# Optimization experiments

Measured on AMD Instinct MI355X. Metric: run time of the kernel, lower is better.

The kernel has to match this reference:

```python
import jax, jax.numpy as jnp
from jax import lax
import numpy as np

B, C, H, W = 32, 128, 64, 64
OUT, KH, KW = 128, 3, 3
E, INTERM = 4, 256


def setup_inputs() -> dict:
    key = jax.random.key(0)
    k1, k2, k3, k4 = jax.random.split(key, 4)
    x = jax.random.normal(k1, (B, C, H, W), dtype=jnp.float32)
    routing_w = jax.random.normal(k2, (INTERM, C), dtype=jnp.float32) * 0.05
    routing_b = jax.random.normal(k3, (INTERM,), dtype=jnp.float32) * 0.05
    expert_weight = jax.random.normal(k4, (E, OUT * C * KH * KW), dtype=jnp.float32) * 0.05
    return {"x": x, "routing_w": routing_w, "routing_b": routing_b, "expert_weight": expert_weight}


def reference(x, routing_w, routing_b, expert_weight):
    b = x.shape[0]
    # adaptive_avg_pool2d(x, 1).flatten(1)
    pooled = x.mean(axis=(2, 3))                              # [B, C]
    rt = jax.nn.sigmoid(pooled @ routing_w.T + routing_b)     # [B, 256]
    # avg_pool1d kernel=stride=interm_d//num_experts
    routing = rt.reshape(b, E, INTERM // E).mean(axis=-1)     # [B, E]
    # CondConv2d: per-sample mixed kernels, grouped conv over batch
    w = routing @ expert_weight                               # [B, OUT*C*KH*KW]
    w = w.reshape(b * OUT, C, KH, KW)                         # OIHW, O grouped by sample
    xg = x.reshape(1, b * C, H, W)
    y = lax.conv_general_dilated(
        xg, w,
        window_strides=(1, 1),
        padding=((1, 1), (1, 1)),
        dimension_numbers=('NCHW', 'OIHW', 'NCHW'),
        feature_group_count=b,
    )
    return y.reshape(b, OUT, H, W)
```

## Files before the change

kernel.cpp:

```cpp
#include <hip/hip_runtime.h>

typedef __attribute__((ext_vector_type(8))) short short8;
typedef __attribute__((ext_vector_type(4))) float f32x4;

#define B_      32
#define C_      128
#define H_      64
#define W_      64
#define OUT_    128
#define PLANE   4096
#define EWSZ    147456

__device__ inline short f2bf(float f) {
    unsigned u = __builtin_bit_cast(unsigned, f);
    u += 0x7fff + ((u >> 16) & 1);
    return (short)(u >> 16);
}

__global__ void pool_kernel(const float* __restrict__ x, float* __restrict__ pooled) {
    const int bc = blockIdx.x;
    const float4* plane = (const float4*)(x + (size_t)bc * PLANE);
    float s = 0.f;
#pragma unroll
    for (int i = 0; i < 4; ++i) {
        float4 v = plane[threadIdx.x + i * 256];
        s += v.x + v.y + v.z + v.w;
    }
#pragma unroll
    for (int off = 32; off > 0; off >>= 1) s += __shfl_down(s, off);
    __shared__ float ls[4];
    const int wave = threadIdx.x >> 6, lane = threadIdx.x & 63;
    if (lane == 0) ls[wave] = s;
    __syncthreads();
    if (threadIdx.x == 0)
        pooled[bc] = (ls[0] + ls[1] + ls[2] + ls[3]) * (1.f / 4096.f);
}

__global__ void routing_kernel(const float* __restrict__ pooled,
                               const float* __restrict__ rw,
                               const float* __restrict__ rb,
                               float* __restrict__ routing) {
    const int b = blockIdx.x;
    __shared__ float ps[C_];
    if (threadIdx.x < C_) ps[threadIdx.x] = pooled[b * C_ + threadIdx.x];
    __syncthreads();
    const int i = threadIdx.x;
    const float4* w4 = (const float4*)(rw + (size_t)i * C_);
    float z = rb[i];
#pragma unroll 8
    for (int c4 = 0; c4 < 32; ++c4) {
        float4 wv = w4[c4];
        z += wv.x * ps[c4 * 4 + 0] + wv.y * ps[c4 * 4 + 1]
           + wv.z * ps[c4 * 4 + 2] + wv.w * ps[c4 * 4 + 3];
    }
    float s = 1.f / (1.f + expf(-z));
#pragma unroll
    for (int off = 32; off > 0; off >>= 1) s += __shfl_down(s, off);
    if ((threadIdx.x & 63) == 0)
        routing[b * 4 + (threadIdx.x >> 6)] = s * (1.f / 64.f);
}

__global__ void wgen_kernel(const float* __restrict__ routing,
                            const float* __restrict__ ew,
                            short* __restrict__ wbuf) {
    const int ct = blockIdx.x;
    const int cc = ct / 9, t = ct % 9;
    const int b = blockIdx.y;
    const int tid = threadIdx.x;
    const int mf = tid >> 6, l = tid & 63;
    const int o = mf * 16 + (l & 15);
    const int c0 = cc * 32 + ((l >> 4) << 3);
    const float r0 = routing[b * 4 + 0], r1 = routing[b * 4 + 1];
    const float r2 = routing[b * 4 + 2], r3 = routing[b * 4 + 3];
    const float* e0 = ew + (size_t)o * 1152 + (size_t)c0 * 9 + t;
    short8 v;
#pragma unroll
    for (int j = 0; j < 8; ++j) {
        const float* p = e0 + j * 9;
        float val = r0 * p[0] + r1 * p[EWSZ] + r2 * p[2 * EWSZ] + r3 * p[3 * EWSZ];
        v[j] = f2bf(val);
    }
    *(short8*)(wbuf + ((size_t)(b * 4 + cc) * 36864 + ((size_t)(t * 8 + mf) * 64 + l) * 8)) = v;
}

__global__ __launch_bounds__(512, 2) void conv_kernel(const float* __restrict__ x,
                                                      const short* __restrict__ wbuf,
                                                      float* __restrict__ out) {
    __shared__ __attribute__((aligned(16))) short ws_s[36864];
    __shared__ __attribute__((aligned(16))) short xs_s[26400];

    const int b = blockIdx.x, hb = blockIdx.y;
    const int h0 = hb * 8;
    const int tid = threadIdx.x;
    const int wid = tid >> 6, lane = tid & 63;
    const int ln15 = lane & 15, lg = lane >> 4;

    for (int i = tid; i < 13200; i += 512) ((int*)xs_s)[i] = 0;

    f32x4 acc[8][4];
#pragma unroll
    for (int m = 0; m < 8; ++m)
#pragma unroll
        for (int n = 0; n < 4; ++n) acc[m][n] = (f32x4){0.f, 0.f, 0.f, 0.f};

    const float* xb = x + (size_t)b * C_ * PLANE;
    const short* wsrc_b = wbuf + (size_t)b * 4 * 36864;

    int tw[5], tr[5], tcg[5], trow[5];
#pragma unroll
    for (int it = 0; it < 5; ++it) {
        const int task = it * 512 + tid;
        tw[it] = task & 63;
        const int rc = task >> 6;
        tr[it] = rc % 10;
        tcg[it] = rc / 10;
        trow[it] = h0 - 1 + tr[it];
    }

    float xpre[5][8];
#pragma unroll
    for (int it = 0; it < 5; ++it) {
        const bool valid = (unsigned)trow[it] < 64u;
        const float* src = xb + (size_t)(tcg[it] * 8) * PLANE + trow[it] * 64 + tw[it];
#pragma unroll
        for (int k = 0; k < 8; ++k)
            xpre[it][k] = valid ? src[(size_t)k * PLANE] : 0.f;
    }

    __syncthreads();

    for (int cc = 0; cc < 4; ++cc) {
#pragma unroll
        for (int it = 0; it < 5; ++it) {
            short8 v;
#pragma unroll
            for (int k = 0; k < 8; ++k) v[k] = f2bf(xpre[it][k]);
            *(short8*)&xs_s[((tr[it] * 66) + 1 + tw[it]) * 40 + tcg[it] * 8] = v;
        }
        {
            const char* srcb = (const char*)(wsrc_b + (size_t)cc * 36864);
            char* dstb = (char*)ws_s;
#pragma unroll
            for (int it = 0; it < 9; ++it) {
                const int off = (wid * 9 + it) * 1024 + lane * 16;
                __builtin_amdgcn_global_load_lds(
                    (const __attribute__((address_space(1))) void*)(srcb + off),
                    (__attribute__((address_space(3))) void*)(dstb + off), 16, 0, 0);
            }
        }
        __syncthreads();

        if (cc < 3) {
#pragma unroll
            for (int it = 0; it < 5; ++it) {
                const bool valid = (unsigned)trow[it] < 64u;
                const float* src = xb + (size_t)((cc + 1) * 32 + tcg[it] * 8) * PLANE
                                 + trow[it] * 64 + tw[it];
#pragma unroll
                for (int k = 0; k < 8; ++k)
                    xpre[it][k] = valid ? src[(size_t)k * PLANE] : 0.f;
            }
        }

#pragma unroll
        for (int t = 0; t < 9; ++t) {
            const int kh = t / 3, kw = t % 3;
            short8 bfr[4];
#pragma unroll
            for (int nf = 0; nf < 4; ++nf)
                bfr[nf] = *(const short8*)&xs_s[(((wid + kh) * 66) + nf * 16 + ln15 + kw) * 40 + lg * 8];
#pragma unroll
            for (int mf = 0; mf < 8; ++mf) {
                short8 af = *(const short8*)&ws_s[((t * 8 + mf) * 64 + lane) * 8];
#pragma unroll
                for (int nf = 0; nf < 4; ++nf)
                    acc[mf][nf] = __builtin_amdgcn_mfma_f32_16x16x32_bf16(
                        af, bfr[nf], acc[mf][nf], 0, 0, 0);
            }
        }
        __syncthreads();
    }

    float* ob = out + (size_t)b * OUT_ * PLANE;
    const int h = h0 + wid;
#pragma unroll
    for (int mf = 0; mf < 8; ++mf) {
#pragma unroll
        for (int nf = 0; nf < 4; ++nf) {
            const int w = nf * 16 + ln15;
            const int o0 = mf * 16 + lg * 4;
#pragma unroll
            for (int q = 0; q < 4; ++q)
                ob[((size_t)(o0 + q) * 64 + h) * 64 + w] = acc[mf][nf][q];
        }
    }
}

extern "C" void kernel_launch(void* const* d_in, const int* in_sizes, int n_in,
                              void* d_out, int out_size, void* d_ws, size_t ws_size,
                              hipStream_t stream) {
    const float* x  = (const float*)d_in[0];
    const float* rw = (const float*)d_in[1];
    const float* rb = (const float*)d_in[2];
    const float* ew = (const float*)d_in[3];
    float* out = (float*)d_out;

    float* pooled  = (float*)d_ws;
    float* routing = pooled + 4096;
    short* wbuf    = (short*)(pooled + 8192);

    pool_kernel<<<dim3(B_ * C_), 256, 0, stream>>>(x, pooled);
    routing_kernel<<<dim3(B_), 256, 0, stream>>>(pooled, rw, rb, routing);
    wgen_kernel<<<dim3(36, B_), 512, 0, stream>>>(routing, ew, wbuf);
    conv_kernel<<<dim3(B_, 8), 512, 0, stream>>>(x, wbuf, out);
}
```

Before: 189.4 us.

## Pre-pack expert weights, vectorize mixing, and shrink conv tiles for occupancy

A new kernel repacks the expert weights into the MFMA fragment layout once. A simpler vectorized mix kernel then blends the four experts per sample with coalesced loads, replacing the strided gather in the old weight generator. The conv kernel moves to 256 threads covering 4 output rows and uses a smaller LDS footprint. It stages the weight tile in two halves (taps 0-3, then 4-8) and converts the x prefetch to bf16 in registers, so more blocks fit per CU and the grid doubles. In exchange it adds an extra kernel launch and workspace traffic, more barriers per channel chunk, and each weight tile is reloaded by twice as many blocks.

After: 197.9 us. +4.5%, slower.

```diff
diff --git a/kernel.cpp b/kernel.cpp
--- a/kernel.cpp
+++ b/kernel.cpp
@@ -1,6 +1,7 @@
 #include <hip/hip_runtime.h>
 
 typedef __attribute__((ext_vector_type(8))) short short8;
+typedef __attribute__((ext_vector_type(4))) short shortv4;
 typedef __attribute__((ext_vector_type(4))) float f32x4;
 
 #define B_      32
@@ -60,42 +61,71 @@
         routing[b * 4 + (threadIdx.x >> 6)] = s * (1.f / 64.f);
 }
 
-__global__ void wgen_kernel(const float* __restrict__ routing,
-                            const float* __restrict__ ew,
+__global__ void epack_kernel(const float* __restrict__ ew, float* __restrict__ epk) {
+    const int os = blockIdx.x;
+    const int cc = blockIdx.y;
+    const int e  = blockIdx.z;
+    __shared__ float ls[16 * 292];
+    const int tid = threadIdx.x;
+
+    for (int idx = tid; idx < 1152; idx += 256) {
+        const int i = idx / 72, q = idx % 72;
+        float4 v = *(const float4*)(ew + (size_t)e * EWSZ
+                     + (size_t)(os * 16 + i) * 1152 + cc * 288 + q * 4);
+        *(float4*)&ls[i * 292 + q * 4] = v;
+    }
+    __syncthreads();
+
+    float* outp = epk + ((size_t)e * 4 + cc) * 36864;
+    for (int idx = tid; idx < 1152; idx += 256) {
+        const int t = idx / 128, r = idx % 128;
+        const int l = r >> 1, j0 = (r & 1) * 4;
+        const int row = l & 15, cb = (l >> 4) * 8 + j0;
+        float4 v;
+        v.x = ls[row * 292 + (cb + 0) * 9 + t];
+        v.y = ls[row * 292 + (cb + 1) * 9 + t];
+        v.z = ls[row * 292 + (cb + 2) * 9 + t];
+        v.w = ls[row * 292 + (cb + 3) * 9 + t];
+        *(float4*)(outp + (size_t)(t * 8 + os) * 512 + r * 4) = v;
+    }
+}
+
+__global__ void wmix_kernel(const float* __restrict__ rbuf,
+                            const float* __restrict__ epk,
                             short* __restrict__ wbuf) {
-    const int ct = blockIdx.x;
-    const int cc = ct / 9, t = ct % 9;
-    const int b = blockIdx.y;
-    const int tid = threadIdx.x;
-    const int mf = tid >> 6, l = tid & 63;
-    const int o = mf * 16 + (l & 15);
-    const int c0 = cc * 32 + ((l >> 4) << 3);
-    const float r0 = routing[b * 4 + 0], r1 = routing[b * 4 + 1];
-    const float r2 = routing[b * 4 + 2], r3 = routing[b * 4 + 3];
-    const float* e0 = ew + (size_t)o * 1152 + (size_t)c0 * 9 + t;
-    short8 v;
-#pragma unroll
-    for (int j = 0; j < 8; ++j) {
-        const float* p = e0 + j * 9;
-        float val = r0 * p[0] + r1 * p[EWSZ] + r2 * p[2 * EWSZ] + r3 * p[3 * EWSZ];
-        v[j] = f2bf(val);
-    }
-    *(short8*)(wbuf + ((size_t)(b * 4 + cc) * 36864 + ((size_t)(t * 8 + mf) * 64 + l) * 8)) = v;
-}
-
-__global__ __launch_bounds__(512, 2) void conv_kernel(const float* __restrict__ x,
+#pragma unroll
+    for (int it = 0; it < 2; ++it) {
+        const int idx = blockIdx.x * 512 + it * 256 + threadIdx.x;
+        const int b = idx / 36864;
+        const int r = idx - b * 36864;
+        const float r0 = rbuf[b * 4 + 0], r1 = rbuf[b * 4 + 1];
+        const float r2 = rbuf[b * 4 + 2], r3 = rbuf[b * 4 + 3];
+        float4 a = *(const float4*)(epk + (size_t)r * 4);
+        float4 bb = *(const float4*)(epk + 147456 + (size_t)r * 4);
+        float4 c = *(const float4*)(epk + 2 * 147456 + (size_t)r * 4);
+        float4 d = *(const float4*)(epk + 3 * 147456 + (size_t)r * 4);
+        shortv4 v;
+        v[0] = f2bf(r0 * a.x + r1 * bb.x + r2 * c.x + r3 * d.x);
+        v[1] = f2bf(r0 * a.y + r1 * bb.y + r2 * c.y + r3 * d.y);
+        v[2] = f2bf(r0 * a.z + r1 * bb.z + r2 * c.z + r3 * d.z);
+        v[3] = f2bf(r0 * a.w + r1 * bb.w + r2 * c.w + r3 * d.w);
+        *(shortv4*)(wbuf + (size_t)b * 147456 + (size_t)r * 4) = v;
+    }
+}
+
+__global__ __launch_bounds__(256, 2) void conv_kernel(const float* __restrict__ x,
                                                       const short* __restrict__ wbuf,
                                                       float* __restrict__ out) {
-    __shared__ __attribute__((aligned(16))) short ws_s[36864];
-    __shared__ __attribute__((aligned(16))) short xs_s[26400];
+    __shared__ __attribute__((aligned(16))) short xs_s[15840];
+    __shared__ __attribute__((aligned(16))) short ws_s[20480];
 
     const int b = blockIdx.x, hb = blockIdx.y;
-    const int h0 = hb * 8;
+    const int h0 = hb * 4;
     const int tid = threadIdx.x;
     const int wid = tid >> 6, lane = tid & 63;
     const int ln15 = lane & 15, lg = lane >> 4;
 
-    for (int i = tid; i < 13200; i += 512) ((int*)xs_s)[i] = 0;
+    for (int i = tid; i < 7920; i += 256) ((int*)xs_s)[i] = 0;
 
     f32x4 acc[8][4];
 #pragma unroll
@@ -106,78 +136,83 @@
     const float* xb = x + (size_t)b * C_ * PLANE;
     const short* wsrc_b = wbuf + (size_t)b * 4 * 36864;
 
-    int tw[5], tr[5], tcg[5], trow[5];
-#pragma unroll
-    for (int it = 0; it < 5; ++it) {
-        const int task = it * 512 + tid;
+    int tw[6], tr[6], tcg[6], trow[6];
+#pragma unroll
+    for (int it = 0; it < 6; ++it) {
+        const int task = it * 256 + tid;
         tw[it] = task & 63;
         const int rc = task >> 6;
-        tr[it] = rc % 10;
-        tcg[it] = rc / 10;
+        tr[it] = rc % 6;
+        tcg[it] = rc / 6;
         trow[it] = h0 - 1 + tr[it];
     }
 
-    float xpre[5][8];
-#pragma unroll
-    for (int it = 0; it < 5; ++it) {
-        const bool valid = (unsigned)trow[it] < 64u;
-        const float* src = xb + (size_t)(tcg[it] * 8) * PLANE + trow[it] * 64 + tw[it];
-#pragma unroll
-        for (int k = 0; k < 8; ++k)
-            xpre[it][k] = valid ? src[(size_t)k * PLANE] : 0.f;
-    }
-
+    short8 xpre[6];
+#define LOADX(CCC)                                                              \
+    {                                                                           \
+        _Pragma("unroll")                                                       \
+        for (int it = 0; it < 6; ++it) {                                        \
+            const bool valid = (unsigned)trow[it] < 64u;                        \
+            const float* src = xb + (size_t)((CCC) * 32 + tcg[it] * 8) * PLANE  \
+                             + trow[it] * 64 + tw[it];                          \
+            short8 v;                                                           \
+            _Pragma("unroll")                                                   \
+            for (int k = 0; k < 8; ++k)                                         \
+                v[k] = f2bf(valid ? src[(size_t)k * PLANE] : 0.f);              \
+            xpre[it] = v;                                                       \
+        }                                                                       \
+    }
+
+#define DO_TAP(TL, T)                                                           \
+    {                                                                           \
+        const int kh = (T) / 3, kw = (T) % 3;                                   \
+        short8 bfr[4];                                                          \
+        _Pragma("unroll")                                                       \
+        for (int nf = 0; nf < 4; ++nf)                                          \
+            bfr[nf] = *(const short8*)&xs_s[((wid + kh) * 66 + nf * 16 + ln15 + kw) * 40 + lg * 8]; \
+        _Pragma("unroll")                                                       \
+        for (int mf = 0; mf < 8; ++mf) {                                        \
+            short8 af = *(const short8*)&ws_s[(((TL) * 8 + mf) * 64 + lane) * 8]; \
+            _Pragma("unroll")                                                   \
+            for (int nf = 0; nf < 4; ++nf)                                      \
+                acc[mf][nf] = __builtin_amdgcn_mfma_f32_16x16x32_bf16(          \
+                    af, bfr[nf], acc[mf][nf], 0, 0, 0);                         \
+        }                                                                       \
+    }
+
+    LOADX(0);
     __syncthreads();
 
     for (int cc = 0; cc < 4; ++cc) {
 #pragma unroll
-        for (int it = 0; it < 5; ++it) {
-            short8 v;
-#pragma unroll
-            for (int k = 0; k < 8; ++k) v[k] = f2bf(xpre[it][k]);
-            *(short8*)&xs_s[((tr[it] * 66) + 1 + tw[it]) * 40 + tcg[it] * 8] = v;
+        for (int it = 0; it < 6; ++it)
+            *(short8*)&xs_s[((tr[it] * 66) + 1 + tw[it]) * 40 + tcg[it] * 8] = xpre[it];
+
+        const char* srcb = (const char*)(wsrc_b + (size_t)cc * 36864);
+#pragma unroll
+        for (int it = 0; it < 8; ++it) {
+            const int off = (wid * 8 + it) * 1024 + lane * 16;
+            __builtin_amdgcn_global_load_lds(
+                (const __attribute__((address_space(1))) void*)(srcb + off),
+                (__attribute__((address_space(3))) void*)(((char*)ws_s) + off), 16, 0, 0);
         }
-        {
-            const char* srcb = (const char*)(wsrc_b + (size_t)cc * 36864);
-            char* dstb = (char*)ws_s;
-#pragma unroll
-            for (int it = 0; it < 9; ++it) {
-                const int off = (wid * 9 + it) * 1024 + lane * 16;
-                __builtin_amdgcn_global_load_lds(
-                    (const __attribute__((address_space(1))) void*)(srcb + off),
-                    (__attribute__((address_space(3))) void*)(dstb + off), 16, 0, 0);
-            }
+        __syncthreads();
+
+        DO_TAP(0, 0) DO_TAP(1, 1) DO_TAP(2, 2) DO_TAP(3, 3)
+        __syncthreads();
+
+#pragma unroll
+        for (int it = 0; it < 10; ++it) {
+            const int off = (wid * 10 + it) * 1024 + lane * 16;
+            __builtin_amdgcn_global_load_lds(
+                (const __attribute__((address_space(1))) void*)(srcb + 32768 + off),
+                (__attribute__((address_space(3))) void*)(((char*)ws_s) + off), 16, 0, 0);
         }
         __syncthreads();
 
-        if (cc < 3) {
-#pragma unroll
-            for (int it = 0; it < 5; ++it) {
-                const bool valid = (unsigned)trow[it] < 64u;
-                const float* src = xb + (size_t)((cc + 1) * 32 + tcg[it] * 8) * PLANE
-                                 + trow[it] * 64 + tw[it];
-#pragma unroll
-                for (int k = 0; k < 8; ++k)
-                    xpre[it][k] = valid ? src[(size_t)k * PLANE] : 0.f;
-            }
-        }
-
-#pragma unroll
-        for (int t = 0; t < 9; ++t) {
-            const int kh = t / 3, kw = t % 3;
-            short8 bfr[4];
-#pragma unroll
-            for (int nf = 0; nf < 4; ++nf)
-                bfr[nf] = *(const short8*)&xs_s[(((wid + kh) * 66) + nf * 16 + ln15 + kw) * 40 + lg * 8];
-#pragma unroll
-            for (int mf = 0; mf < 8; ++mf) {
-                short8 af = *(const short8*)&ws_s[((t * 8 + mf) * 64 + lane) * 8];
-#pragma unroll
-                for (int nf = 0; nf < 4; ++nf)
-                    acc[mf][nf] = __builtin_amdgcn_mfma_f32_16x16x32_bf16(
-                        af, bfr[nf], acc[mf][nf], 0, 0, 0);
-            }
-        }
+        if (cc < 3) LOADX(cc + 1);
+
+        DO_TAP(0, 4) DO_TAP(1, 5) DO_TAP(2, 6) DO_TAP(3, 7) DO_TAP(4, 8)
         __syncthreads();
     }
 
@@ -194,6 +229,8 @@
                 ob[((size_t)(o0 + q) * 64 + h) * 64 + w] = acc[mf][nf][q];
         }
     }
+#undef LOADX
+#undef DO_TAP
 }
 
 extern "C" void kernel_launch(void* const* d_in, const int* in_sizes, int n_in,
@@ -207,10 +244,12 @@
 
     float* pooled  = (float*)d_ws;
     float* routing = pooled + 4096;
-    short* wbuf    = (short*)(pooled + 8192);
-
+    float* epk     = pooled + 8192;
+    short* wbuf    = (short*)(epk + 589824);
+
+    epack_kernel<<<dim3(8, 4, 4), 256, 0, stream>>>(ew, epk);
     pool_kernel<<<dim3(B_ * C_), 256, 0, stream>>>(x, pooled);
     routing_kernel<<<dim3(B_), 256, 0, stream>>>(pooled, rw, rb, routing);
-    wgen_kernel<<<dim3(36, B_), 512, 0, stream>>>(routing, ew, wbuf);
-    conv_kernel<<<dim3(B_, 8), 512, 0, stream>>>(x, wbuf, out);
-}
+    wmix_kernel<<<dim3(2304), 256, 0, stream>>>(routing, epk, wbuf);
+    conv_kernel<<<dim3(B_, 16), 256, 0, stream>>>(x, wbuf, out);
+}
```
